# Optimization experiments

Measured on AMD Instinct MI355X. Metric: run time of the kernel, lower is better.

Reference implementation:

```python
import jax, jax.numpy as jnp
import numpy as np
import math

H, D, DEG = 8, 64, 2
GATE_BIAS = 6.906768

def _rope(x, sin, cos):
    # GPT-J style interleaved rotary: even lanes = x1*cos - x2*sin, odd = x2*cos + x1*sin
    x1, x2 = x[..., ::2], x[..., 1::2]
    s = sin[None, :, None, :]
    c = cos[None, :, None, :]
    even = x1 * c - x2 * s
    odd = x2 * c + x1 * s
    return jnp.stack([even, odd], axis=-1).reshape(x.shape)

def _forward(x, w_attn, w_proj):
    B, T, C = x.shape
    h, d, deg = H, D, DEG
    hd = h * d
    scale = 1.0 / math.sqrt(d)
    qkvg = x @ w_attn                                   # (B,T,3hd+h)
    q = qkvg[..., :hd].reshape(B, T, h, d)
    k = qkvg[..., hd:2 * hd].reshape(B, T, h, d)
    v = qkvg[..., 2 * hd:3 * hd].reshape(B, T, h, d)
    log_g = jax.nn.log_sigmoid(GATE_BIAS + qkvg[..., 3 * hd:].astype(jnp.float32))  # (B,T,h)
    # sinusoidal RoPE with frequency 2*pi / T**(2i/d), as in get_sinusoidal_embeddings
    pos = jnp.arange(T, dtype=jnp.float32)
    div = 2.0 * math.pi / (float(T) ** (jnp.arange(0, d, 2, dtype=jnp.float32) / d))
    ang = pos[:, None] * div[None, :]                   # (T, d//2)
    sin, cos = jnp.sin(ang), jnp.cos(ang)
    q = _rope(q, sin, cos)
    k = _rope(k, sin, cos)
    # gated symmetric-power attention: quadratic reference of chunked power_full
    # score_ts = (scale * q_t . k_s)^deg * exp(L_t - L_s), causal, row-normalized
    L = jnp.cumsum(log_g, axis=1).transpose(0, 2, 1)    # (B,h,T) cumulative log-gates
    qk = jnp.einsum('bthd,bshd->bhts', q, k) * scale    # (B,h,T,T)
    log_gate = L[:, :, :, None] - L[:, :, None, :]      # L_t - L_s
    causal = jnp.tril(jnp.ones((T, T), dtype=bool))
    scores = jnp.where(causal, (qk ** deg) * jnp.exp(log_gate), 0.0)
    denom = jnp.maximum(scores.sum(-1, keepdims=True), 1e-6)
    y = jnp.einsum('bhts,bshd->bthd', scores / denom, v)  # (B,T,h,d)
    return y.reshape(B, T, hd) @ w_proj

def setup_inputs() -> dict:
    key = jax.random.key(0)
    k1, k2, k3 = jax.random.split(key, 3)
    B, T, C = 2, 2048, 512
    x = jax.random.normal(k1, (B, T, C), dtype=jnp.float32)
    w_attn = jax.random.normal(k2, (C, 3 * H * D + H), dtype=jnp.float32) * 0.02
    w_proj = jax.random.normal(k3, (H * D, C), dtype=jnp.float32) * 0.02
    return {"x": x, "w_attn": w_attn, "w_proj": w_proj}

def reference(x, w_attn, w_proj):
    return _forward(x, w_attn, w_proj)
```

## Files before the change

kernel.cpp:

```cpp
#include <hip/hip_runtime.h>
#include <hip/hip_bf16.h>
#include <math.h>

constexpr int B_ = 2, T_ = 2048, C_ = 512, H_ = 8, D_ = 64;
constexpr int QKVG_ = 3 * H_ * D_ + H_;
constexpr float GATE_BIAS_ = 6.906768f;
constexpr int N1_ = 1536;
constexpr int SC_ = 8;
constexpr int NBLK_ = 1280;
constexpr int MC_ = 4096 * 512;
constexpr int BHT_ = B_ * H_ * T_;

typedef __attribute__((ext_vector_type(8))) short short8;
typedef __attribute__((ext_vector_type(4))) float f32x4;

__device__ __forceinline__ unsigned short f2b(float f) {
    union { __hip_bfloat16 h; unsigned short u; } cv;
    cv.h = __float2bfloat16(f);
    return cv.u;
}
__device__ __forceinline__ float b2f(unsigned short u) {
    return __uint_as_float((unsigned int)u << 16);
}
__device__ __forceinline__ short8 pack8(float4 a, float4 b) {
    short8 r;
    r[0] = (short)f2b(a.x); r[1] = (short)f2b(a.y);
    r[2] = (short)f2b(a.z); r[3] = (short)f2b(a.w);
    r[4] = (short)f2b(b.x); r[5] = (short)f2b(b.y);
    r[6] = (short)f2b(b.z); r[7] = (short)f2b(b.w);
    return r;
}

__device__ __forceinline__ void gl2lds16(const unsigned short* g, void* lds_base) {
    __builtin_amdgcn_global_load_lds(
        (const __attribute__((address_space(1))) unsigned int*)g,
        (__attribute__((address_space(3))) unsigned int*)lds_base, 16, 0, 0);
}

__device__ __forceinline__ void packT_body(
    const float* __restrict__ W, unsigned short* __restrict__ Bt,
    int K, int N, int ldW, int nt, int kt, int tid, float (*Ws)[65])
{
    {
        const int r = tid >> 2;
        const int c0 = (tid & 3) * 16;
#pragma unroll
        for (int j = 0; j < 16; ++j) {
            const int n = nt + c0 + j;
            Ws[r][c0 + j] = (n < N) ? W[(size_t)(kt + r) * ldW + n] : 0.f;
        }
    }
    __syncthreads();
    {
        const int d = tid >> 2;
        const int cc = tid & 3;
        const int kc = cc * 16;
        short8 o0, o1;
#pragma unroll
        for (int j = 0; j < 8; ++j) o0[j] = (short)f2b(Ws[kc + j][d]);
#pragma unroll
        for (int j = 0; j < 8; ++j) o1[j] = (short)f2b(Ws[kc + 8 + j][d]);
        const int row = nt + d;
        unsigned short* op = Bt + (size_t)row * K + kt;
        *(short8*)(op + ((2 * cc) ^ (row & 7)) * 8)     = o0;
        *(short8*)(op + ((2 * cc + 1) ^ (row & 7)) * 8) = o1;
    }
}

__global__ __launch_bounds__(256) void pack_inputs(
    const float* __restrict__ x, const float* __restrict__ w_attn,
    const float* __restrict__ w_proj, unsigned short* __restrict__ xb,
    unsigned short* __restrict__ Bt1, unsigned short* __restrict__ Bt2,
    float2* __restrict__ sincos, float* __restrict__ g)
{
    __shared__ float SM[64 * 65];
    float (*Ws)[65] = (float(*)[65])SM;
    const int bid = blockIdx.x;
    const int tid = threadIdx.x;
    if (bid < 1024) {
        const int i = bid * 256 + tid;
        float4 f0 = *(const float4*)(x + (size_t)i * 8);
        float4 f1 = *(const float4*)(x + (size_t)i * 8 + 4);
        const int row = i >> 6;
        const int ic = i & 63;
        const int swc = (ic & ~7) | ((ic & 7) ^ (row & 7));
        *(short8*)(xb + (size_t)row * 512 + swc * 8) = pack8(f0, f1);
    } else if (bid < 1216) {
        const int q = bid - 1024;
        packT_body(w_attn, Bt1, C_, N1_, QKVG_, (q % 24) * 64, (q / 24) * 64, tid, Ws);
    } else if (bid < 1280) {
        const int q = bid - 1216;
        packT_body(w_proj, Bt2, H_ * D_, C_, C_, (q & 7) * 64, (q >> 3) * 64, tid, Ws);
    } else if (bid < 1288) {
        const int t = (bid - 1280) * 256 + tid;
        float2* op = sincos + (size_t)t * 32;
#pragma unroll
        for (int i = 0; i < 32; ++i) {
            const float div = 6.2831853071795864f * exp2f((float)i * (-11.0f / 32.0f));
            const float ang = (float)t * div;
            op[i] = make_float2(cosf(ang), sinf(ang));
        }
    } else {
        const int q = bid - 1288;
        float* LDSw = SM;
        {
            const int k = tid * 2;
#pragma unroll
            for (int kk = 0; kk < 2; ++kk) {
                const float* wp = w_attn + (size_t)(k + kk) * QKVG_ + 1536;
                float4 wa = *(const float4*)wp;
                float4 wb = *(const float4*)(wp + 4);
                float* dst = LDSw + (k + kk) * 8;
                *(float4*)dst = wa;
                *(float4*)(dst + 4) = wb;
            }
        }
        __syncthreads();
        const int m = q * 32 + (tid >> 3);
        const int h = tid & 7;
        const float* xrow = x + (size_t)m * C_;
        float s = 0.f;
#pragma unroll 4
        for (int k0 = 0; k0 < 512; k0 += 4) {
            float4 xv = *(const float4*)(xrow + k0);
            s += xv.x * LDSw[(k0 + 0) * 8 + h] + xv.y * LDSw[(k0 + 1) * 8 + h]
               + xv.z * LDSw[(k0 + 2) * 8 + h] + xv.w * LDSw[(k0 + 3) * 8 + h];
        }
        const int b = m >> 11, t = m & 2047;
        g[(size_t)(b * 8 + h) * T_ + t] = s;
    }
}

__global__ __launch_bounds__(256) void gate_cumsum(
    const float* __restrict__ g, float* __restrict__ Lg)
{
    __shared__ float wsum[4];
    const int bh = blockIdx.x;
    const int tid = threadIdx.x;
    const int lane = tid & 63, wv = tid >> 6;

    const float* gp = g + (size_t)bh * T_ + tid * 8;
    float v[8];
    float s = 0.f;
#pragma unroll
    for (int j = 0; j < 8; ++j) {
        const float z = gp[j] + GATE_BIAS_;
        const float lg = (z > 0.f) ? -log1pf(expf(-z)) : (z - log1pf(expf(z)));
        s += lg;
        v[j] = s;
    }
    float ssum = s;
#pragma unroll
    for (int off = 1; off < 64; off <<= 1) {
        float n = __shfl_up(ssum, off, 64);
        if (lane >= off) ssum += n;
    }
    if (lane == 63) wsum[wv] = ssum;
    __syncthreads();
    float base = ssum - s;
#pragma unroll
    for (int w = 0; w < 3; ++w)
        base += (w < wv) ? wsum[w] : 0.f;

    float* op = Lg + (size_t)bh * T_ + tid * 8;
#pragma unroll
    for (int j = 0; j < 8; ++j) op[j] = v[j] + base;
}

__global__ __launch_bounds__(256) void gemm_fused(
    const unsigned short* __restrict__ A, const unsigned short* __restrict__ Bt,
    const float* __restrict__ Lg, const float2* __restrict__ sincos,
    unsigned short* __restrict__ Qsb, unsigned short* __restrict__ Ksb,
    unsigned short* __restrict__ Vtb)
{
    __shared__ __align__(16) char smem[65536];
    float (*epi)[65] = (float(*)[65])smem;

    const int tid = threadIdx.x;
    const int wave = tid >> 6, lane = tid & 63;
    const int l15 = lane & 15, lhi = lane >> 4;
    const int wr = wave >> 1, wc = wave & 1;
    const int bm = blockIdx.y * 128, bn = blockIdx.x * 128;

    f32x4 acc[4][4];
#pragma unroll
    for (int i = 0; i < 4; ++i)
#pragma unroll
        for (int j = 0; j < 4; ++j) acc[i][j] = (f32x4){0.f, 0.f, 0.f, 0.f};

    const unsigned short* Arow = A + (size_t)bm * C_;
    const unsigned short* Brow = Bt + (size_t)bn * C_;
    const int sw = (l15 & 7) << 4;
    const int srow = tid >> 3;
    const int schunk = tid & 7;

#pragma unroll
    for (int p = 0; p < 4; ++p) {
        const int row = p * 32 + srow;
        const size_t goff = (size_t)row * C_ + schunk * 8;
        gl2lds16(Arow + goff, smem + p * 4096 + wave * 1024);
        gl2lds16(Brow + goff, smem + 16384 + p * 4096 + wave * 1024);
    }

    for (int ks = 0; ks < 8; ++ks) {
        __syncthreads();
        if (ks < 7) {
            char* dst = smem + ((ks + 1) & 1) * 32768;
            const int k1 = (ks + 1) * 64;
#pragma unroll
            for (int p = 0; p < 4; ++p) {
                const int row = p * 32 + srow;
                const size_t goff = (size_t)row * C_ + k1 + schunk * 8;
                gl2lds16(Arow + goff, dst + p * 4096 + wave * 1024);
                gl2lds16(Brow + goff, dst + 16384 + p * 4096 + wave * 1024);
            }
        }
        const char* AsB = smem + (ks & 1) * 32768;
        const char* BsB = AsB + 16384;

        short8 af[4][2];
#pragma unroll
        for (int mi = 0; mi < 4; ++mi) {
            const int row = wr * 64 + mi * 16 + l15;
#pragma unroll
            for (int kk = 0; kk < 2; ++kk)
                af[mi][kk] = *(const short8*)(AsB + row * 128 + ((kk * 64 + lhi * 16) ^ sw));
        }
#pragma unroll
        for (int ni = 0; ni < 4; ++ni) {
            const int row = wc * 64 + ni * 16 + l15;
            short8 bf0 = *(const short8*)(BsB + row * 128 + ((lhi * 16) ^ sw));
            short8 bf1 = *(const short8*)(BsB + row * 128 + ((64 + lhi * 16) ^ sw));
#pragma unroll
            for (int mi = 0; mi < 4; ++mi) {
                acc[mi][ni] = __builtin_amdgcn_mfma_f32_16x16x32_bf16(af[mi][0], bf0, acc[mi][ni], 0, 0, 0);
                acc[mi][ni] = __builtin_amdgcn_mfma_f32_16x16x32_bf16(af[mi][1], bf1, acc[mi][ni], 0, 0, 0);
            }
        }
    }

    const int rid = bn >> 9;
    const int b = bm >> 11;
    const int tloc0 = bm & 2047;

#pragma unroll
    for (int hc = 0; hc < 2; ++hc) {
        __syncthreads();
        if (wc == hc) {
#pragma unroll
            for (int mi = 0; mi < 4; ++mi)
#pragma unroll
                for (int ni = 0; ni < 4; ++ni)
#pragma unroll
                    for (int r = 0; r < 4; ++r)
                        epi[wr * 64 + mi * 16 + lhi * 4 + r][ni * 16 + l15] = acc[mi][ni][r];
        }
        __syncthreads();
        const int h = ((bn & 511) >> 6) + hc;
        const int bh = b * 8 + h;
        if (rid < 2) {
            const int row = tid >> 1;
            const int c0 = (tid & 1) * 32;
            const int t = tloc0 + row;
            const float Lt = Lg[(size_t)bh * T_ + t];
            const float scl = (rid == 0) ? (__expf(0.5f * Lt) * 0.125f)
                                         : __expf(-0.5f * Lt);
            float vb[32];
#pragma unroll
            for (int j = 0; j < 32; ++j) vb[j] = epi[row][c0 + j];
            const float2* sct = sincos + (size_t)t * 32 + (c0 >> 1);
#pragma unroll
            for (int p = 0; p < 16; ++p) {
                const float2 cssn = sct[p];
                const float x1 = vb[2 * p], x2 = vb[2 * p + 1];
                vb[2 * p]     = (x1 * cssn.x - x2 * cssn.y) * scl;
                vb[2 * p + 1] = (x2 * cssn.x + x1 * cssn.y) * scl;
            }
            unsigned short* op = ((rid == 0) ? Qsb : Ksb) + ((size_t)bh * T_ + t) * 64;
#pragma unroll
            for (int j = 0; j < 4; ++j) {
                short8 o = pack8(*(float4*)&vb[j * 8], *(float4*)&vb[j * 8 + 4]);
                const int chunk = (c0 >> 3) + j;
                const int pos = (rid == 0) ? chunk : (chunk ^ (t & 7));
                *(short8*)(op + pos * 8) = o;
            }
        } else {
            const int d = tid >> 2;
            const int tq = tid & 3;
            unsigned short* op = Vtb + ((size_t)(bh * 64 + d)) * T_;
#pragma unroll
            for (int j = 0; j < 4; ++j) {
                const int tl = tq * 32 + j * 8;
                short8 o;
#pragma unroll
                for (int e = 0; e < 8; ++e)
                    o[e] = (short)f2b(epi[tl + e][d]);
                const int chunkidx = (tloc0 + tl) >> 3;
                const int pos = (chunkidx & ~7) | ((chunkidx & 7) ^ (d & 7));
                *(short8*)(op + pos * 8) = o;
            }
        }
    }
}

__global__ __launch_bounds__(256) void gemm_bf16(
    const unsigned short* __restrict__ A, const unsigned short* __restrict__ Bt,
    float* __restrict__ C, int M, int N, int K)
{
    __shared__ __align__(16) char smem[49152];

    const int tid = threadIdx.x;
    const int wave = tid >> 6, lane = tid & 63;
    const int l15 = lane & 15, lhi = lane >> 4;
    const int wr = wave >> 1, wc = wave & 1;
    const int bm = blockIdx.y * 64, bn = blockIdx.x * 128;

    f32x4 acc[2][4];
#pragma unroll
    for (int i = 0; i < 2; ++i)
#pragma unroll
        for (int j = 0; j < 4; ++j) acc[i][j] = (f32x4){0.f, 0.f, 0.f, 0.f};

    const unsigned short* Arow = A + (size_t)bm * K;
    const unsigned short* Brow = Bt + (size_t)bn * K;
    const int sw = (l15 & 7) << 4;
    const int srow = tid >> 3;
    const int schunk = tid & 7;
    const int nks = K >> 6;

#pragma unroll
    for (int p = 0; p < 2; ++p) {
        const int row = p * 32 + srow;
        gl2lds16(Arow + (size_t)row * K + schunk * 8, smem + p * 4096 + wave * 1024);
    }
#pragma unroll
    for (int p = 0; p < 4; ++p) {
        const int row = p * 32 + srow;
        gl2lds16(Brow + (size_t)row * K + schunk * 8, smem + 8192 + p * 4096 + wave * 1024);
    }

    for (int ks = 0; ks < nks; ++ks) {
        __syncthreads();
        if (ks + 1 < nks) {
            char* dst = smem + ((ks + 1) & 1) * 24576;
            const int k1 = (ks + 1) * 64;
#pragma unroll
            for (int p = 0; p < 2; ++p) {
                const int row = p * 32 + srow;
                gl2lds16(Arow + (size_t)row * K + k1 + schunk * 8, dst + p * 4096 + wave * 1024);
            }
#pragma unroll
            for (int p = 0; p < 4; ++p) {
                const int row = p * 32 + srow;
                gl2lds16(Brow + (size_t)row * K + k1 + schunk * 8, dst + 8192 + p * 4096 + wave * 1024);
            }
        }
        const char* AsB = smem + (ks & 1) * 24576;
        const char* BsB = AsB + 8192;

        short8 af[2][2];
#pragma unroll
        for (int mi = 0; mi < 2; ++mi) {
            const int row = wr * 32 + mi * 16 + l15;
#pragma unroll
            for (int kk = 0; kk < 2; ++kk)
                af[mi][kk] = *(const short8*)(AsB + row * 128 + ((kk * 64 + lhi * 16) ^ sw));
        }
#pragma unroll
        for (int ni = 0; ni < 4; ++ni) {
            const int row = wc * 64 + ni * 16 + l15;
            short8 bf0 = *(const short8*)(BsB + row * 128 + ((lhi * 16) ^ sw));
            short8 bf1 = *(const short8*)(BsB + row * 128 + ((64 + lhi * 16) ^ sw));
#pragma unroll
            for (int mi = 0; mi < 2; ++mi) {
                acc[mi][ni] = __builtin_amdgcn_mfma_f32_16x16x32_bf16(af[mi][0], bf0, acc[mi][ni], 0, 0, 0);
                acc[mi][ni] = __builtin_amdgcn_mfma_f32_16x16x32_bf16(af[mi][1], bf1, acc[mi][ni], 0, 0, 0);
            }
        }
    }

#pragma unroll
    for (int mi = 0; mi < 2; ++mi) {
        const int gm = bm + wr * 32 + mi * 16 + lhi * 4;
#pragma unroll
        for (int r = 0; r < 4; ++r) {
            float* crow = C + (size_t)(gm + r) * N;
#pragma unroll
            for (int ni = 0; ni < 4; ++ni) {
                const int gn = bn + wc * 64 + ni * 16 + l15;
                if (gn < N) crow[gn] = acc[mi][ni][r];
            }
        }
    }
}

__global__ __launch_bounds__(256) void attn_mfma(
    const unsigned short* __restrict__ Qsb, const unsigned short* __restrict__ Ksb,
    const unsigned short* __restrict__ Vtb,
    unsigned short* __restrict__ Ypb, float* __restrict__ Dpart)
{
    __shared__ __align__(16) char smem[40960];
    char* PsB = smem + 32768;

    const int wg = blockIdx.x;
    const int xcd = wg & 7;
    const int slot = wg >> 3;
    const int bh = (slot < 80) ? xcd : 8 + xcd;
    const int rem = (slot < 80) ? slot : slot - 80;
    const int rr = 79 - rem;
    int bt, sc;
    if (rr < 8)       { bt = rr; sc = 0; }
    else if (rr < 24) { const int q = rr - 8;  bt = 8 + (q >> 1);  sc = q & 1; }
    else if (rr < 48) { const int q = rr - 24; bt = 16 + q / 3;    sc = q % 3; }
    else              { const int q = rr - 48; bt = 24 + (q >> 2); sc = q & 3; }
    const int st0 = sc * SC_;
    const int st1 = min(st0 + SC_ - 1, bt);

    const int tid = threadIdx.x;
    const int wave = tid >> 6;
    const int lane = tid & 63;
    const int l15 = lane & 15;
    const int lhi = lane >> 4;
    const int b = bh >> 3, h = bh & 7;
    const int t0 = bt * 64;

    const int qrow = t0 + wave * 16 + l15;
    const unsigned short* qpp = Qsb + ((size_t)bh * T_ + qrow) * 64 + lhi * 8;
    short8 qf[2];
    qf[0] = *(const short8*)(qpp);
    qf[1] = *(const short8*)(qpp + 32);

    f32x4 accY[4];
#pragma unroll
    for (int n = 0; n < 4; ++n) accY[n] = (f32x4){0.f, 0.f, 0.f, 0.f};
    float den[4] = {0.f, 0.f, 0.f, 0.f};

    const int kchunk = lhi * 16;
    const int rsw = (l15 & 7) << 4;
    const int srow = tid >> 3;
    const int schunk = tid & 7;

#pragma unroll
    for (int p = 0; p < 2; ++p) {
        const int row = p * 32 + srow;
        gl2lds16(Ksb + ((size_t)bh * T_ + st0 * 64 + row) * 64 + schunk * 8,
                 smem + p * 4096 + wave * 1024);
        gl2lds16(Vtb + ((size_t)bh * 64 + row) * T_ + st0 * 64 + schunk * 8,
                 smem + 8192 + p * 4096 + wave * 1024);
    }

    for (int st = st0; st <= st1; ++st) {
        __syncthreads();
        if (st < st1) {
            char* dst = smem + (((st - st0) + 1) & 1) * 16384;
            const int s1 = (st + 1) * 64;
#pragma unroll
            for (int p = 0; p < 2; ++p) {
                const int row = p * 32 + srow;
                gl2lds16(Ksb + ((size_t)bh * T_ + s1 + row) * 64 + schunk * 8,
                         dst + p * 4096 + wave * 1024);
                gl2lds16(Vtb + ((size_t)bh * 64 + row) * T_ + s1 + schunk * 8,
                         dst + 8192 + p * 4096 + wave * 1024);
            }
        }
        const char* KsB = smem + ((st - st0) & 1) * 16384;
        const char* VtB = KsB + 8192;

        f32x4 accS[4];
#pragma unroll
        for (int n = 0; n < 4; ++n) accS[n] = (f32x4){0.f, 0.f, 0.f, 0.f};
        __builtin_amdgcn_s_setprio(1);
#pragma unroll
        for (int n = 0; n < 4; ++n) {
#pragma unroll
            for (int kk = 0; kk < 2; ++kk) {
                short8 bf = *(const short8*)(KsB + (n * 16 + l15) * 128 + ((kk * 64 + kchunk) ^ rsw));
                accS[n] = __builtin_amdgcn_mfma_f32_16x16x32_bf16(qf[kk], bf, accS[n], 0, 0, 0);
            }
        }
        __builtin_amdgcn_s_setprio(0);

        const bool last = (st == bt);
        char* PsW = PsB + wave * 2048;
#pragma unroll
        for (int n = 0; n < 4; ++n) {
#pragma unroll
            for (int r = 0; r < 4; ++r) {
                const float a = accS[n][r];
                float p = a * a;
                if (last)
                    p = ((n * 16 + l15) <= wave * 16 + lhi * 4 + r) ? p : 0.f;
                den[r] += p;
                const int prow = lhi * 4 + r;
                *(unsigned short*)(PsW + prow * 128 + ((2 * (n * 16 + l15)) ^ ((prow & 7) << 4))) = f2b(p);
            }
        }

        short8 pa[2];
#pragma unroll
        for (int kk = 0; kk < 2; ++kk)
            pa[kk] = *(const short8*)(PsW + l15 * 128 + ((kk * 64 + kchunk) ^ rsw));
        __builtin_amdgcn_s_setprio(1);
#pragma unroll
        for (int n = 0; n < 4; ++n) {
#pragma unroll
            for (int kk = 0; kk < 2; ++kk) {
                short8 vb = *(const short8*)(VtB + (n * 16 + l15) * 128 + ((kk * 64 + kchunk) ^ rsw));
                accY[n] = __builtin_amdgcn_mfma_f32_16x16x32_bf16(pa[kk], vb, accY[n], 0, 0, 0);
            }
        }
        __builtin_amdgcn_s_setprio(0);
    }

#pragma unroll
    for (int r = 0; r < 4; ++r) {
        den[r] += __shfl_xor(den[r], 1, 64);
        den[r] += __shfl_xor(den[r], 2, 64);
        den[r] += __shfl_xor(den[r], 4, 64);
        den[r] += __shfl_xor(den[r], 8, 64);
    }

    unsigned short* Ybase = Ypb + (size_t)sc * MC_;
    float* Dbase = Dpart + (size_t)sc * BHT_;
#pragma unroll
    for (int r = 0; r < 4; ++r) {
        const int t = t0 + wave * 16 + lhi * 4 + r;
        if (l15 == 0)
            Dbase[(size_t)bh * T_ + t] = den[r];
        unsigned short* yo = Ybase + (size_t)(b * T_ + t) * (H_ * D_) + h * 64 + l15;
#pragma unroll
        for (int n = 0; n < 4; ++n)
            yo[n * 16] = f2b(accY[n][r]);
    }
}

__global__ __launch_bounds__(256) void normalize_kernel(
    const unsigned short* __restrict__ Ypb, const float* __restrict__ Dpart,
    unsigned short* __restrict__ ybb)
{
    const int gid = blockIdx.x * 256 + threadIdx.x;
    const size_t base = (size_t)gid * 8;
    const int row = (int)(base >> 9);
    const int col = (int)(base & 511);
    const int b = row >> 11, t = row & 2047, h = col >> 6;
    const int bh = b * H_ + h;
    const int nsc = (t >> 9) + 1;

    float acc[8] = {0.f, 0.f, 0.f, 0.f, 0.f, 0.f, 0.f, 0.f};
    float d = 0.f;
    for (int s = 0; s < nsc; ++s) {
        d += Dpart[(size_t)s * BHT_ + (size_t)bh * T_ + t];
        short8 v = *(const short8*)(Ypb + (size_t)s * MC_ + base);
#pragma unroll
        for (int j = 0; j < 8; ++j)
            acc[j] += b2f((unsigned short)v[j]);
    }
    const float inv = 1.0f / fmaxf(d, 1e-6f);
    float4 f0 = make_float4(acc[0] * inv, acc[1] * inv, acc[2] * inv, acc[3] * inv);
    float4 f1 = make_float4(acc[4] * inv, acc[5] * inv, acc[6] * inv, acc[7] * inv);

    const int ic = col >> 3;
    const int swc = (ic & ~7) | ((ic & 7) ^ (row & 7));
    *(short8*)(ybb + (size_t)row * 512 + swc * 8) = pack8(f0, f1);
}

extern "C" void kernel_launch(void* const* d_in, const int* in_sizes, int n_in,
                              void* d_out, int out_size, void* d_ws, size_t ws_size,
                              hipStream_t stream)
{
    const float* x      = (const float*)d_in[0];
    const float* w_attn = (const float*)d_in[1];
    const float* w_proj = (const float*)d_in[2];
    float* out = (float*)d_out;

    char* p = (char*)d_ws;
    float2* sincos = (float2*)p;               p += (size_t)T_ * 32 * 8;
    float* g       = (float*)p;                p += (size_t)BHT_ * 4;
    float* Lg      = (float*)p;                p += (size_t)BHT_ * 4;
    float* Dpart   = (float*)p;                p += (size_t)4 * BHT_ * 4;
    unsigned short* xb  = (unsigned short*)p;  p += (size_t)MC_ * 2;
    unsigned short* Bt1 = (unsigned short*)p;  p += (size_t)N1_ * C_ * 2;
    unsigned short* Bt2 = (unsigned short*)p;  p += (size_t)C_ * C_ * 2;
    unsigned short* Qsb = (unsigned short*)p;  p += (size_t)BHT_ * 64 * 2;
    unsigned short* Ksb = (unsigned short*)p;  p += (size_t)BHT_ * 64 * 2;
    unsigned short* Vtb = (unsigned short*)p;  p += (size_t)BHT_ * 64 * 2;
    unsigned short* Ypb = (unsigned short*)p;  p += (size_t)4 * MC_ * 2;
    unsigned short* ybb = (unsigned short*)p;

    const int M = B_ * T_;

    pack_inputs<<<1416, 256, 0, stream>>>(x, w_attn, w_proj, xb, Bt1, Bt2, sincos, g);

    gate_cumsum<<<B_ * H_, 256, 0, stream>>>(g, Lg);

    gemm_fused<<<dim3(N1_ / 128, M / 128), 256, 0, stream>>>(
        xb, Bt1, Lg, sincos, Qsb, Ksb, Vtb);

    attn_mfma<<<NBLK_, 256, 0, stream>>>(Qsb, Ksb, Vtb, Ypb, Dpart);

    normalize_kernel<<<(MC_ / 8) / 256, 256, 0, stream>>>(Ypb, Dpart, ybb);

    gemm_bf16<<<dim3(C_ / 128, M / 64), 256, 0, stream>>>(
        ybb, Bt2, out, M, C_, H_ * D_);
}
```

Measured before the change: 76.53 us.

## Fuse partial-sum normalization into the output projection GEMM prologue

Removes the separate normalize kernel and the ybb intermediate buffer. The output-projection GEMM now reads the split-chunk partial Y tiles and denominators directly, sums and normalizes them in registers, and writes the bf16 A tile into swizzled LDS. It prefetches the next tile's partials into registers while the current tile's MFMAs run. This saves one launch and a full write/read round trip of the normalized activations. In exchange, each of the 4 N-column blocks re-reads and re-reduces the same partials, and register pressure rises from holding up to 4 prefetched partial vectors.

```diff
diff --git a/kernel.cpp b/kernel.cpp
--- a/kernel.cpp
+++ b/kernel.cpp
@@ -303,97 +303,6 @@
     }
 }
 
-__global__ __launch_bounds__(256) void gemm_bf16(
-    const unsigned short* __restrict__ A, const unsigned short* __restrict__ Bt,
-    float* __restrict__ C, int M, int N, int K)
-{
-    __shared__ __align__(16) char smem[49152];
-
-    const int tid = threadIdx.x;
-    const int wave = tid >> 6, lane = tid & 63;
-    const int l15 = lane & 15, lhi = lane >> 4;
-    const int wr = wave >> 1, wc = wave & 1;
-    const int bm = blockIdx.y * 64, bn = blockIdx.x * 128;
-
-    f32x4 acc[2][4];
-#pragma unroll
-    for (int i = 0; i < 2; ++i)
-#pragma unroll
-        for (int j = 0; j < 4; ++j) acc[i][j] = (f32x4){0.f, 0.f, 0.f, 0.f};
-
-    const unsigned short* Arow = A + (size_t)bm * K;
-    const unsigned short* Brow = Bt + (size_t)bn * K;
-    const int sw = (l15 & 7) << 4;
-    const int srow = tid >> 3;
-    const int schunk = tid & 7;
-    const int nks = K >> 6;
-
-#pragma unroll
-    for (int p = 0; p < 2; ++p) {
-        const int row = p * 32 + srow;
-        gl2lds16(Arow + (size_t)row * K + schunk * 8, smem + p * 4096 + wave * 1024);
-    }
-#pragma unroll
-    for (int p = 0; p < 4; ++p) {
-        const int row = p * 32 + srow;
-        gl2lds16(Brow + (size_t)row * K + schunk * 8, smem + 8192 + p * 4096 + wave * 1024);
-    }
-
-    for (int ks = 0; ks < nks; ++ks) {
-        __syncthreads();
-        if (ks + 1 < nks) {
-            char* dst = smem + ((ks + 1) & 1) * 24576;
-            const int k1 = (ks + 1) * 64;
-#pragma unroll
-            for (int p = 0; p < 2; ++p) {
-                const int row = p * 32 + srow;
-                gl2lds16(Arow + (size_t)row * K + k1 + schunk * 8, dst + p * 4096 + wave * 1024);
-            }
-#pragma unroll
-            for (int p = 0; p < 4; ++p) {
-                const int row = p * 32 + srow;
-                gl2lds16(Brow + (size_t)row * K + k1 + schunk * 8, dst + 8192 + p * 4096 + wave * 1024);
-            }
-        }
-        const char* AsB = smem + (ks & 1) * 24576;
-        const char* BsB = AsB + 8192;
-
-        short8 af[2][2];
-#pragma unroll
-        for (int mi = 0; mi < 2; ++mi) {
-            const int row = wr * 32 + mi * 16 + l15;
-#pragma unroll
-            for (int kk = 0; kk < 2; ++kk)
-                af[mi][kk] = *(const short8*)(AsB + row * 128 + ((kk * 64 + lhi * 16) ^ sw));
-        }
-#pragma unroll
-        for (int ni = 0; ni < 4; ++ni) {
-            const int row = wc * 64 + ni * 16 + l15;
-            short8 bf0 = *(const short8*)(BsB + row * 128 + ((lhi * 16) ^ sw));
-            short8 bf1 = *(const short8*)(BsB + row * 128 + ((64 + lhi * 16) ^ sw));
-#pragma unroll
-            for (int mi = 0; mi < 2; ++mi) {
-                acc[mi][ni] = __builtin_amdgcn_mfma_f32_16x16x32_bf16(af[mi][0], bf0, acc[mi][ni], 0, 0, 0);
-                acc[mi][ni] = __builtin_amdgcn_mfma_f32_16x16x32_bf16(af[mi][1], bf1, acc[mi][ni], 0, 0, 0);
-            }
-        }
-    }
-
-#pragma unroll
-    for (int mi = 0; mi < 2; ++mi) {
-        const int gm = bm + wr * 32 + mi * 16 + lhi * 4;
-#pragma unroll
-        for (int r = 0; r < 4; ++r) {
-            float* crow = C + (size_t)(gm + r) * N;
-#pragma unroll
-            for (int ni = 0; ni < 4; ++ni) {
-                const int gn = bn + wc * 64 + ni * 16 + l15;
-                if (gn < N) crow[gn] = acc[mi][ni][r];
-            }
-        }
-    }
-}
-
 __global__ __launch_bounds__(256) void attn_mfma(
     const unsigned short* __restrict__ Qsb, const unsigned short* __restrict__ Ksb,
     const unsigned short* __restrict__ Vtb,
@@ -534,34 +443,150 @@
     }
 }
 
-__global__ __launch_bounds__(256) void normalize_kernel(
+__global__ __launch_bounds__(256) void gemm2_fused(
     const unsigned short* __restrict__ Ypb, const float* __restrict__ Dpart,
-    unsigned short* __restrict__ ybb)
+    const unsigned short* __restrict__ Bt, float* __restrict__ C)
 {
-    const int gid = blockIdx.x * 256 + threadIdx.x;
-    const size_t base = (size_t)gid * 8;
-    const int row = (int)(base >> 9);
-    const int col = (int)(base & 511);
-    const int b = row >> 11, t = row & 2047, h = col >> 6;
-    const int bh = b * H_ + h;
-    const int nsc = (t >> 9) + 1;
-
-    float acc[8] = {0.f, 0.f, 0.f, 0.f, 0.f, 0.f, 0.f, 0.f};
-    float d = 0.f;
-    for (int s = 0; s < nsc; ++s) {
-        d += Dpart[(size_t)s * BHT_ + (size_t)bh * T_ + t];
-        short8 v = *(const short8*)(Ypb + (size_t)s * MC_ + base);
-#pragma unroll
-        for (int j = 0; j < 8; ++j)
-            acc[j] += b2f((unsigned short)v[j]);
-    }
-    const float inv = 1.0f / fmaxf(d, 1e-6f);
-    float4 f0 = make_float4(acc[0] * inv, acc[1] * inv, acc[2] * inv, acc[3] * inv);
-    float4 f1 = make_float4(acc[4] * inv, acc[5] * inv, acc[6] * inv, acc[7] * inv);
-
-    const int ic = col >> 3;
-    const int swc = (ic & ~7) | ((ic & 7) ^ (row & 7));
-    *(short8*)(ybb + (size_t)row * 512 + swc * 8) = pack8(f0, f1);
+    __shared__ __align__(16) char smem[51200];
+    float* invden = (float*)(smem + 49152);
+
+    const int tid = threadIdx.x;
+    const int wave = tid >> 6, lane = tid & 63;
+    const int l15 = lane & 15, lhi = lane >> 4;
+    const int wr = wave >> 1, wc = wave & 1;
+    const int bm = blockIdx.y * 64, bn = blockIdx.x * 128;
+    const int b = bm >> 11, t0 = bm & 2047;
+    const int nsc = (t0 >> 9) + 1;
+
+#pragma unroll
+    for (int q = 0; q < 2; ++q) {
+        const int idx = q * 256 + tid;
+        const int h = idx >> 6, row = idx & 63;
+        float d = 0.f;
+        for (int s = 0; s < nsc; ++s)
+            d += Dpart[(size_t)s * BHT_ + (size_t)(b * 8 + h) * T_ + t0 + row];
+        invden[idx] = 1.0f / fmaxf(d, 1e-6f);
+    }
+
+    const unsigned short* Brow = Bt + (size_t)bn * C_;
+    const int sw = (l15 & 7) << 4;
+    const int srow = tid >> 3;
+    const int schunk = tid & 7;
+
+    f32x4 acc[2][4];
+#pragma unroll
+    for (int i = 0; i < 2; ++i)
+#pragma unroll
+        for (int j = 0; j < 4; ++j) acc[i][j] = (f32x4){0.f, 0.f, 0.f, 0.f};
+
+#pragma unroll
+    for (int p = 0; p < 4; ++p) {
+        const int row = p * 32 + srow;
+        gl2lds16(Brow + (size_t)row * C_ + schunk * 8, smem + 8192 + p * 4096 + wave * 1024);
+    }
+    __syncthreads();
+
+#pragma unroll
+    for (int p = 0; p < 2; ++p) {
+        const int row = p * 32 + srow;
+        float a8[8] = {0.f, 0.f, 0.f, 0.f, 0.f, 0.f, 0.f, 0.f};
+#pragma unroll
+        for (int s = 0; s < 4; ++s) {
+            if (s < nsc) {
+                short8 v = *(const short8*)(Ypb + (size_t)s * MC_ + (size_t)(bm + row) * 512 + schunk * 8);
+#pragma unroll
+                for (int j = 0; j < 8; ++j) a8[j] += b2f((unsigned short)v[j]);
+            }
+        }
+        const float iv = invden[row];
+#pragma unroll
+        for (int j = 0; j < 8; ++j) a8[j] *= iv;
+        short8 o = pack8(*(float4*)&a8[0], *(float4*)&a8[4]);
+        *(short8*)(smem + row * 128 + ((schunk << 4) ^ ((row & 7) << 4))) = o;
+    }
+
+    for (int ks = 0; ks < 8; ++ks) {
+        __syncthreads();
+        short8 vv[2][4];
+        const bool have = (ks < 7);
+        if (have) {
+            char* dst = smem + ((ks + 1) & 1) * 24576;
+            const int k1 = (ks + 1) * 64;
+#pragma unroll
+            for (int p = 0; p < 4; ++p) {
+                const int row = p * 32 + srow;
+                gl2lds16(Brow + (size_t)row * C_ + k1 + schunk * 8, dst + 8192 + p * 4096 + wave * 1024);
+            }
+#pragma unroll
+            for (int p = 0; p < 2; ++p) {
+                const int row = p * 32 + srow;
+#pragma unroll
+                for (int s = 0; s < 4; ++s) {
+                    if (s < nsc)
+                        vv[p][s] = *(const short8*)(Ypb + (size_t)s * MC_ + (size_t)(bm + row) * 512 + k1 + schunk * 8);
+                    else
+                        vv[p][s] = (short8){0,0,0,0,0,0,0,0};
+                }
+            }
+        }
+
+        const char* AsB = smem + (ks & 1) * 24576;
+        const char* BsB = AsB + 8192;
+
+        short8 af[2][2];
+#pragma unroll
+        for (int mi = 0; mi < 2; ++mi) {
+            const int row = wr * 32 + mi * 16 + l15;
+#pragma unroll
+            for (int kk = 0; kk < 2; ++kk)
+                af[mi][kk] = *(const short8*)(AsB + row * 128 + ((kk * 64 + lhi * 16) ^ sw));
+        }
+#pragma unroll
+        for (int ni = 0; ni < 4; ++ni) {
+            const int row = wc * 64 + ni * 16 + l15;
+            short8 bf0 = *(const short8*)(BsB + row * 128 + ((lhi * 16) ^ sw));
+            short8 bf1 = *(const short8*)(BsB + row * 128 + ((64 + lhi * 16) ^ sw));
+#pragma unroll
+            for (int mi = 0; mi < 2; ++mi) {
+                acc[mi][ni] = __builtin_amdgcn_mfma_f32_16x16x32_bf16(af[mi][0], bf0, acc[mi][ni], 0, 0, 0);
+                acc[mi][ni] = __builtin_amdgcn_mfma_f32_16x16x32_bf16(af[mi][1], bf1, acc[mi][ni], 0, 0, 0);
+            }
+        }
+
+        if (have) {
+            char* dst = smem + ((ks + 1) & 1) * 24576;
+            const int h1 = ks + 1;
+#pragma unroll
+            for (int p = 0; p < 2; ++p) {
+                const int row = p * 32 + srow;
+                float a8[8] = {0.f, 0.f, 0.f, 0.f, 0.f, 0.f, 0.f, 0.f};
+#pragma unroll
+                for (int s = 0; s < 4; ++s) {
+#pragma unroll
+                    for (int j = 0; j < 8; ++j) a8[j] += b2f((unsigned short)vv[p][s][j]);
+                }
+                const float iv = invden[h1 * 64 + row];
+#pragma unroll
+                for (int j = 0; j < 8; ++j) a8[j] *= iv;
+                short8 o = pack8(*(float4*)&a8[0], *(float4*)&a8[4]);
+                *(short8*)(dst + row * 128 + ((schunk << 4) ^ ((row & 7) << 4))) = o;
+            }
+        }
+    }
+
+#pragma unroll
+    for (int mi = 0; mi < 2; ++mi) {
+        const int gm = bm + wr * 32 + mi * 16 + lhi * 4;
+#pragma unroll
+        for (int r = 0; r < 4; ++r) {
+            float* crow = C + (size_t)(gm + r) * C_;
+#pragma unroll
+            for (int ni = 0; ni < 4; ++ni) {
+                const int gn = bn + wc * 64 + ni * 16 + l15;
+                crow[gn] = acc[mi][ni][r];
+            }
+        }
+    }
 }
 
 extern "C" void kernel_launch(void* const* d_in, const int* in_sizes, int n_in,
@@ -584,8 +609,7 @@
     unsigned short* Qsb = (unsigned short*)p;  p += (size_t)BHT_ * 64 * 2;
     unsigned short* Ksb = (unsigned short*)p;  p += (size_t)BHT_ * 64 * 2;
     unsigned short* Vtb = (unsigned short*)p;  p += (size_t)BHT_ * 64 * 2;
-    unsigned short* Ypb = (unsigned short*)p;  p += (size_t)4 * MC_ * 2;
-    unsigned short* ybb = (unsigned short*)p;
+    unsigned short* Ypb = (unsigned short*)p;
 
     const int M = B_ * T_;
 
@@ -598,8 +622,6 @@
 
     attn_mfma<<<NBLK_, 256, 0, stream>>>(Qsb, Ksb, Vtb, Ypb, Dpart);
 
-    normalize_kernel<<<(MC_ / 8) / 256, 256, 0, stream>>>(Ypb, Dpart, ybb);
-
-    gemm_bf16<<<dim3(C_ / 128, M / 64), 256, 0, stream>>>(
-        ybb, Bt2, out, M, C_, H_ * D_);
-}
+    gemm2_fused<<<dim3(C_ / 128, M / 64), 256, 0, stream>>>(
+        Ypb, Dpart, Bt2, out);
+}
```

After: 79.25 us. +3.6%, slower.
